# Optimization experiments

Measured on AMD Instinct MI355X. Metric: run time of the kernel, lower is better.

Reference implementation:

```python
import jax, jax.numpy as jnp
import numpy as np

D_IN = 64      # num_in_features
D_OUT = 64     # num_out_features
H = 512        # neurons_per_layer
M = 64         # num_meta_in_features
META_OUT = D_IN * H + H + H * D_OUT + D_OUT  # 66112
B = 2048


def setup_inputs() -> dict:
    key = jax.random.key(0)
    k1, k2, k3 = jax.random.split(key, 3)
    x = jax.random.normal(k1, (B, D_IN + M), dtype=jnp.float32)
    # xavier-normal-ish init for the two hypernet linears, zero biases
    W_in = jax.random.normal(k2, (H, M), dtype=jnp.float32) * jnp.sqrt(2.0 / (H + M))
    b_in = jnp.zeros((H,), dtype=jnp.float32)
    W_out = jax.random.normal(k3, (META_OUT, H), dtype=jnp.float32) * jnp.sqrt(2.0 / (META_OUT + H))
    b_out = jnp.zeros((META_OUT,), dtype=jnp.float32)
    return {"x": x, "W_in": W_in, "b_in": b_in, "W_out": W_out, "b_out": b_out}


def reference(x, W_in, b_in, W_out, b_out):
    real = x[:, :D_IN]            # [B, D_IN]
    meta = x[:, D_IN:]            # [B, M]
    h = jax.nn.elu(meta @ W_in.T + b_in)          # [B, H]
    gen = h @ W_out.T + b_out                     # [B, META_OUT]
    base = D_IN * H
    l_in_w = gen[:, :base].reshape(-1, D_IN, H)   # [B, D_IN, H]
    l_in_b = gen[:, base:base + H]                # [B, H]
    base += H
    add = H * D_OUT
    l_out_w = gen[:, base:base + add].reshape(-1, H, D_OUT)  # [B, H, D_OUT]
    l_out_b = gen[:, base + add:]                 # [B, D_OUT]
    # tensordot(real, l_in_w, dims=([1],[1])).diagonal(0,1).T == per-sample matvec
    y = jax.nn.elu(jnp.einsum('bi,bih->bh', real, l_in_w) + l_in_b)
    out = jnp.einsum('bh,bho->bo', y, l_out_w) + l_out_b
    return out
```

## Files before the change

kernel.cpp:

```cpp
#include <hip/hip_runtime.h>
#include <hip/hip_bf16.h>
#include <stdint.h>

#define B_N   2048
#define XW    128
#define KDIM  512
#define NROWS_W   66112
#define NROWS_PAD 66560

typedef __bf16 v8bf  __attribute__((ext_vector_type(8)));
typedef float  f32x4 __attribute__((ext_vector_type(4)));

__device__ __forceinline__ unsigned short f2bf(float f) {
    uint32_t u = __float_as_uint(f);
    u += 0x7FFF + ((u >> 16) & 1);
    return (unsigned short)(u >> 16);
}
__device__ __forceinline__ float elu1(float v) {
    return v > 0.0f ? v : expm1f(v);
}
__device__ __forceinline__ void gload_lds16(const void* g, void* l) {
    __builtin_amdgcn_global_load_lds(
        (const __attribute__((address_space(1))) unsigned int*)g,
        (__attribute__((address_space(3))) unsigned int*)l, 16, 0, 0);
}

__global__ void k_h(const float* __restrict__ x, const float* __restrict__ W_in,
                    const float* __restrict__ b_in, unsigned short* __restrict__ hb) {
    int idx = blockIdx.x * 256 + threadIdx.x;
    int b = idx >> 9, j = idx & 511;
    const float4* xm = (const float4*)(x + (size_t)b * XW + 64);
    const float4* wr = (const float4*)(W_in + (size_t)j * 64);
    float acc = 0.f;
#pragma unroll
    for (int q = 0; q < 16; ++q) {
        float4 a = xm[q], w = wr[q];
        acc += a.x * w.x + a.y * w.y + a.z * w.z + a.w * w.w;
    }
    acc = elu1(acc + b_in[j]);
    hb[idx] = f2bf(acc);
}

__global__ void k_conv(const float* __restrict__ Wf, unsigned short* __restrict__ Wb) {
    size_t c = (size_t)blockIdx.x * 256 + threadIdx.x;
    size_t row = c >> 6; int kk = (int)(c & 63);
    union { uint4 v; unsigned short u[8]; } o;
    o.v = (uint4){0, 0, 0, 0};
    if (row < NROWS_W) {
        const float* wp = Wf + row * KDIM + kk * 8;
        float4 w0 = *(const float4*)wp, w1 = *(const float4*)(wp + 4);
        o.u[0] = f2bf(w0.x); o.u[1] = f2bf(w0.y); o.u[2] = f2bf(w0.z); o.u[3] = f2bf(w0.w);
        o.u[4] = f2bf(w1.x); o.u[5] = f2bf(w1.y); o.u[6] = f2bf(w1.z); o.u[7] = f2bf(w1.w);
    }
    *(uint4*)(Wb + c * 8) = o.v;
}

template<int MODE>
__global__ __launch_bounds__(256, 2)
void k_pgemm(const unsigned short* __restrict__ hb,
             const unsigned short* __restrict__ Wb,
             const float* __restrict__ scaleSrc,
             float* __restrict__ outAcc) {
    constexpr int NP   = MODE ? 129 : 130;
    constexpr int OUTW = MODE ? 64 : 512;
    constexpr int SCW  = MODE ? 18 : 9;

    __shared__ char smem[65536 + SCW * 128 * 4];
    char* As = smem;
    char* Bs = smem + 32768;
    float* sc = (float*)(smem + 65536);

    const int tid = threadIdx.x;
    const int m0  = blockIdx.x * 128;
    const int nh  = blockIdx.y;
    const int s   = blockIdx.z;
    const int pBeg = (NP * s) >> 4;
    const int pEnd = (NP * (s + 1)) >> 4;
    const int halfS = (MODE == 0 && pBeg >= 65) ? 1 : 0;
    const int iBeg  = pBeg - halfS * 65;

    const int wid = tid >> 6, l = tid & 63;
    const int lr = l & 15, lg = l >> 4;
    const int wm = wid >> 1, wn = wid & 1;

    for (int c = tid; c < SCW * 128; c += 256) {
        int jj = c >> 7, row = c & 127;
        float v = 1.0f;
        if (MODE == 0) {
            int i = iBeg + jj;
            if (i < 64) v = scaleSrc[(size_t)(m0 + row) * XW + i];
        } else {
            int g = (pBeg + (jj >> 1)) * 4 + nh * 2 + (jj & 1);
            if (g < 512) v = scaleSrc[(size_t)(m0 + row) * KDIM + g];
        }
        sc[c] = v;
    }

    int aB[4], aX[4], bB[4], bX[4];
#pragma unroll
    for (int q = 0; q < 4; ++q) {
        int ra = wm * 64 + q * 16 + lr;
        aB[q] = ra * 256; aX[q] = ra & 7;
        int rb = wn * 64 + q * 16 + lr;
        bB[q] = rb * 128; bX[q] = rb & 7;
    }

    f32x4 accP[4][4], accO[4][4];
#pragma unroll
    for (int mi = 0; mi < 4; ++mi)
#pragma unroll
        for (int ni = 0; ni < 4; ++ni) {
            accP[mi][ni] = (f32x4){0.f, 0.f, 0.f, 0.f};
            accO[mi][ni] = (f32x4){0.f, 0.f, 0.f, 0.f};
        }

    for (int kq = 0; kq < 4; ++kq) {
#pragma unroll
        for (int q = 0; q < 8; ++q) {
            int c = q * 256 + tid;
            int row = c >> 4, kk = c & 15;
            uint4 v = *(const uint4*)(hb + (size_t)(m0 + row) * KDIM + kq * 128 + kk * 8);
            *(uint4*)(As + row * 256 + ((kk ^ (row & 7)) << 4)) = v;
        }
        auto stageB = [&](int buf, int p, int k0c) {
            int wrow = MODE ? (33280 + p * 256 + nh * 128)
                            : ((p - halfS * 65) * 512 + halfS * 256 + nh * 128);
            const int rsub = tid >> 3;
            const int sl = (tid & 7) ^ (rsub & 7);
            const unsigned short* src0 = Wb + (size_t)(wrow + rsub) * KDIM
                                       + kq * 128 + k0c * 64 + sl * 8;
            char* dst0 = Bs + buf * 16384 + tid * 16;
#pragma unroll
            for (int q = 0; q < 4; ++q)
                gload_lds16(src0 + (size_t)q * 32 * KDIM, dst0 + q * 4096);
        };
        stageB(0, pBeg, 0);
        __syncthreads();
        int cur = 0;
        for (int p = pBeg; p < pEnd; ++p) {
#pragma unroll
            for (int k0 = 0; k0 < 2; ++k0) {
                const bool last = (p == pEnd - 1) && (k0 == 1);
                if (!last) {
                    stageB(cur ^ 1, k0 ? p + 1 : p, k0 ^ 1);
                    asm volatile("s_waitcnt vmcnt(4)" ::: "memory");
                } else {
                    asm volatile("s_waitcnt vmcnt(0)" ::: "memory");
                }
                __builtin_amdgcn_s_barrier();
                asm volatile("" ::: "memory");
                char* Bbuf = Bs + cur * 16384;
                __builtin_amdgcn_s_setprio(1);
#pragma unroll
                for (int ks = 0; ks < 2; ++ks) {
                    v8bf af[4], bfr[4];
                    const int sA = k0 * 8 + ks * 4 + lg;
                    const int sB = ks * 4 + lg;
#pragma unroll
                    for (int mi = 0; mi < 4; ++mi)
                        af[mi] = *(const v8bf*)(As + aB[mi] + ((sA ^ aX[mi]) << 4));
#pragma unroll
                    for (int ni = 0; ni < 4; ++ni)
                        bfr[ni] = *(const v8bf*)(Bbuf + bB[ni] + ((sB ^ bX[ni]) << 4));
#pragma unroll
                    for (int mi = 0; mi < 4; ++mi)
#pragma unroll
                        for (int ni = 0; ni < 4; ++ni)
                            accP[mi][ni] = __builtin_amdgcn_mfma_f32_16x16x32_bf16(
                                af[mi], bfr[ni], accP[mi][ni], 0, 0, 0);
                }
                __builtin_amdgcn_s_setprio(0);
                if (k0 == 1) {
                    int jj = MODE ? ((p - pBeg) * 2 + wn) : (p - pBeg);
                    const f32x4* scv = (const f32x4*)(sc + jj * 128);
#pragma unroll
                    for (int mi = 0; mi < 4; ++mi) {
                        f32x4 sv = scv[wm * 16 + mi * 4 + lg];
#pragma unroll
                        for (int ni = 0; ni < 4; ++ni) {
                            accO[mi][ni] += sv * accP[mi][ni];
                            accP[mi][ni] = (f32x4){0.f, 0.f, 0.f, 0.f};
                        }
                    }
                }
                asm volatile("" ::: "memory");
                __builtin_amdgcn_s_barrier();
                cur ^= 1;
            }
        }
    }
#pragma unroll
    for (int mi = 0; mi < 4; ++mi)
#pragma unroll
        for (int ni = 0; ni < 4; ++ni)
#pragma unroll
            for (int r = 0; r < 4; ++r) {
                int row = wm * 64 + mi * 16 + lg * 4 + r;
                int col = MODE ? (ni * 16 + lr)
                               : (halfS * 256 + nh * 128 + wn * 64 + ni * 16 + lr);
                atomicAdd(outAcc + (size_t)(m0 + row) * OUTW + col, accO[mi][ni][r]);
            }
}

__global__ void k_fin_y(const float* __restrict__ ypre, const float* __restrict__ x,
                        const float* __restrict__ b_out, float* __restrict__ y) {
    int idx = blockIdx.x * 256 + threadIdx.x;
    int b = idx >> 9, hh = idx & 511;
    float acc = ypre[idx] + b_out[32768 + hh];
    const float* xr = x + (size_t)b * XW;
#pragma unroll 8
    for (int i = 0; i < 64; ++i)
        acc += xr[i] * b_out[i * 512 + hh];
    y[idx] = elu1(acc);
}

__global__ void k_fin_out(const float* __restrict__ y, const float* __restrict__ b_out,
                          float* __restrict__ out) {
    int idx = blockIdx.x * 256 + threadIdx.x;
    int b = idx >> 6, o = idx & 63;
    float acc = out[idx] + b_out[66048 + o];
    const float* yr = y + (size_t)b * 512;
#pragma unroll 8
    for (int hh = 0; hh < 512; ++hh)
        acc += yr[hh] * b_out[33280 + hh * 64 + o];
    out[idx] = acc;
}

extern "C" void kernel_launch(void* const* d_in, const int* in_sizes, int n_in,
                              void* d_out, int out_size, void* d_ws, size_t ws_size,
                              hipStream_t stream) {
    const float* x     = (const float*)d_in[0];
    const float* W_in  = (const float*)d_in[1];
    const float* b_in  = (const float*)d_in[2];
    const float* W_out = (const float*)d_in[3];
    const float* b_out = (const float*)d_in[4];
    float* out = (float*)d_out;

    char* ws = (char*)d_ws;
    unsigned short* hb = (unsigned short*)ws;
    float* ypre        = (float*)(ws + (2u << 20));
    float* yv          = (float*)(ws + (6u << 20));
    unsigned short* Wb = (unsigned short*)(ws + (10u << 20));

    hipMemsetAsync(ypre, 0, (size_t)B_N * 512 * 4, stream);
    hipMemsetAsync(out,  0, (size_t)B_N * 64 * 4, stream);

    k_h<<<(B_N * 512) / 256, 256, 0, stream>>>(x, W_in, b_in, hb);
    k_conv<<<(NROWS_PAD * KDIM / 8) / 256, 256, 0, stream>>>(W_out, Wb);

    k_pgemm<0><<<dim3(16, 2, 16), 256, 0, stream>>>(hb, Wb, x, ypre);

    k_fin_y<<<(B_N * 512) / 256, 256, 0, stream>>>(ypre, x, b_out, yv);

    k_pgemm<1><<<dim3(16, 2, 16), 256, 0, stream>>>(hb, Wb, yv, out);

    k_fin_out<<<(B_N * 64) / 256, 256, 0, stream>>>(yv, b_out, out);
}
```

Measured before the change: 284.4 us.

## Hold A fragments in registers, enlarge M tile, fold bias terms into init kernels

The projected GEMM now uses 512-thread blocks covering 256 rows. Each wave loads its A (h) fragments straight from global memory into registers once per k-quarter instead of staging them through LDS. This halves LDS use and doubles reuse of each streamed W tile. The grid is flattened to 256 blocks with a custom mapping of split index to block. The memsets and the two finalize kernels are replaced by init kernels that write the bias contributions before the atomics, and ELU is applied on the fly when scales are loaded and inside k_init_out. The cost is higher register pressure and direct global A loads without LDS swizzling.

```diff
diff --git a/kernel.cpp b/kernel.cpp
--- a/kernel.cpp
+++ b/kernel.cpp
@@ -55,8 +55,32 @@
     *(uint4*)(Wb + c * 8) = o.v;
 }
 
+__global__ void k_init_ypre(const float* __restrict__ x, const float* __restrict__ b_out,
+                            float* __restrict__ ypre) {
+    int idx = blockIdx.x * 256 + threadIdx.x;
+    int b = idx >> 9, hh = idx & 511;
+    float acc = b_out[32768 + hh];
+    const float* xr = x + (size_t)b * XW;
+#pragma unroll 8
+    for (int i = 0; i < 64; ++i)
+        acc += xr[i] * b_out[i * 512 + hh];
+    ypre[idx] = acc;
+}
+
+__global__ void k_init_out(const float* __restrict__ ypre, const float* __restrict__ b_out,
+                           float* __restrict__ out) {
+    int idx = blockIdx.x * 256 + threadIdx.x;
+    int b = idx >> 6, o = idx & 63;
+    float acc = b_out[66048 + o];
+    const float* yr = ypre + (size_t)b * 512;
+#pragma unroll 4
+    for (int hh = 0; hh < 512; ++hh)
+        acc += elu1(yr[hh]) * b_out[33280 + hh * 64 + o];
+    out[idx] = acc;
+}
+
 template<int MODE>
-__global__ __launch_bounds__(256, 2)
+__global__ __launch_bounds__(512, 2)
 void k_pgemm(const unsigned short* __restrict__ hb,
              const unsigned short* __restrict__ Wb,
              const float* __restrict__ scaleSrc,
@@ -65,42 +89,42 @@
     constexpr int OUTW = MODE ? 64 : 512;
     constexpr int SCW  = MODE ? 18 : 9;
 
-    __shared__ char smem[65536 + SCW * 128 * 4];
-    char* As = smem;
-    char* Bs = smem + 32768;
-    float* sc = (float*)(smem + 65536);
-
-    const int tid = threadIdx.x;
-    const int m0  = blockIdx.x * 128;
-    const int nh  = blockIdx.y;
-    const int s   = blockIdx.z;
+    __shared__ char smem[32768 + SCW * 256 * 4];
+    char* Bs = smem;
+    float* sc = (float*)(smem + 32768);
+
+    const int lid = blockIdx.x;
+    const int s   = (lid & 7) * 2 + (lid >> 7);
+    const int inner = (lid >> 3) & 15;
+    const int m0  = (inner & 7) * 256;
+    const int nh  = inner >> 3;
+
     const int pBeg = (NP * s) >> 4;
     const int pEnd = (NP * (s + 1)) >> 4;
     const int halfS = (MODE == 0 && pBeg >= 65) ? 1 : 0;
     const int iBeg  = pBeg - halfS * 65;
 
+    const int tid = threadIdx.x;
     const int wid = tid >> 6, l = tid & 63;
     const int lr = l & 15, lg = l >> 4;
     const int wm = wid >> 1, wn = wid & 1;
 
-    for (int c = tid; c < SCW * 128; c += 256) {
-        int jj = c >> 7, row = c & 127;
+    for (int c = tid; c < SCW * 256; c += 512) {
+        int jj = c >> 8, row = c & 255;
         float v = 1.0f;
         if (MODE == 0) {
             int i = iBeg + jj;
             if (i < 64) v = scaleSrc[(size_t)(m0 + row) * XW + i];
         } else {
             int g = (pBeg + (jj >> 1)) * 4 + nh * 2 + (jj & 1);
-            if (g < 512) v = scaleSrc[(size_t)(m0 + row) * KDIM + g];
+            if (g < 512) v = elu1(scaleSrc[(size_t)(m0 + row) * KDIM + g]);
         }
         sc[c] = v;
     }
 
-    int aB[4], aX[4], bB[4], bX[4];
+    int bB[4], bX[4];
 #pragma unroll
     for (int q = 0; q < 4; ++q) {
-        int ra = wm * 64 + q * 16 + lr;
-        aB[q] = ra * 256; aX[q] = ra & 7;
         int rb = wn * 64 + q * 16 + lr;
         bB[q] = rb * 128; bX[q] = rb & 7;
     }
@@ -115,13 +139,6 @@
         }
 
     for (int kq = 0; kq < 4; ++kq) {
-#pragma unroll
-        for (int q = 0; q < 8; ++q) {
-            int c = q * 256 + tid;
-            int row = c >> 4, kk = c & 15;
-            uint4 v = *(const uint4*)(hb + (size_t)(m0 + row) * KDIM + kq * 128 + kk * 8);
-            *(uint4*)(As + row * 256 + ((kk ^ (row & 7)) << 4)) = v;
-        }
         auto stageB = [&](int buf, int p, int k0c) {
             int wrow = MODE ? (33280 + p * 256 + nh * 128)
                             : ((p - halfS * 65) * 512 + halfS * 256 + nh * 128);
@@ -131,11 +148,21 @@
                                        + kq * 128 + k0c * 64 + sl * 8;
             char* dst0 = Bs + buf * 16384 + tid * 16;
 #pragma unroll
-            for (int q = 0; q < 4; ++q)
-                gload_lds16(src0 + (size_t)q * 32 * KDIM, dst0 + q * 4096);
+            for (int q = 0; q < 2; ++q)
+                gload_lds16(src0 + (size_t)q * 64 * KDIM, dst0 + q * 8192);
         };
+
         stageB(0, pBeg, 0);
-        __syncthreads();
+
+        const unsigned short* abase = hb + (size_t)(m0 + wm * 64 + lr) * KDIM
+                                    + kq * 128 + lg * 8;
+        v8bf areg[4][4];
+#pragma unroll
+        for (int mi = 0; mi < 4; ++mi)
+#pragma unroll
+            for (int kk2 = 0; kk2 < 4; ++kk2)
+                areg[mi][kk2] = *(const v8bf*)(abase + mi * 16 * KDIM + kk2 * 32);
+
         int cur = 0;
         for (int p = pBeg; p < pEnd; ++p) {
 #pragma unroll
@@ -143,7 +170,7 @@
                 const bool last = (p == pEnd - 1) && (k0 == 1);
                 if (!last) {
                     stageB(cur ^ 1, k0 ? p + 1 : p, k0 ^ 1);
-                    asm volatile("s_waitcnt vmcnt(4)" ::: "memory");
+                    asm volatile("s_waitcnt vmcnt(2)" ::: "memory");
                 } else {
                     asm volatile("s_waitcnt vmcnt(0)" ::: "memory");
                 }
@@ -153,12 +180,8 @@
                 __builtin_amdgcn_s_setprio(1);
 #pragma unroll
                 for (int ks = 0; ks < 2; ++ks) {
-                    v8bf af[4], bfr[4];
-                    const int sA = k0 * 8 + ks * 4 + lg;
+                    v8bf bfr[4];
                     const int sB = ks * 4 + lg;
-#pragma unroll
-                    for (int mi = 0; mi < 4; ++mi)
-                        af[mi] = *(const v8bf*)(As + aB[mi] + ((sA ^ aX[mi]) << 4));
 #pragma unroll
                     for (int ni = 0; ni < 4; ++ni)
                         bfr[ni] = *(const v8bf*)(Bbuf + bB[ni] + ((sB ^ bX[ni]) << 4));
@@ -167,12 +190,12 @@
 #pragma unroll
                         for (int ni = 0; ni < 4; ++ni)
                             accP[mi][ni] = __builtin_amdgcn_mfma_f32_16x16x32_bf16(
-                                af[mi], bfr[ni], accP[mi][ni], 0, 0, 0);
+                                areg[mi][k0 * 2 + ks], bfr[ni], accP[mi][ni], 0, 0, 0);
                 }
                 __builtin_amdgcn_s_setprio(0);
                 if (k0 == 1) {
                     int jj = MODE ? ((p - pBeg) * 2 + wn) : (p - pBeg);
-                    const f32x4* scv = (const f32x4*)(sc + jj * 128);
+                    const f32x4* scv = (const f32x4*)(sc + jj * 256);
 #pragma unroll
                     for (int mi = 0; mi < 4; ++mi) {
                         f32x4 sv = scv[wm * 16 + mi * 4 + lg];
@@ -202,30 +225,6 @@
             }
 }
 
-__global__ void k_fin_y(const float* __restrict__ ypre, const float* __restrict__ x,
-                        const float* __restrict__ b_out, float* __restrict__ y) {
-    int idx = blockIdx.x * 256 + threadIdx.x;
-    int b = idx >> 9, hh = idx & 511;
-    float acc = ypre[idx] + b_out[32768 + hh];
-    const float* xr = x + (size_t)b * XW;
-#pragma unroll 8
-    for (int i = 0; i < 64; ++i)
-        acc += xr[i] * b_out[i * 512 + hh];
-    y[idx] = elu1(acc);
-}
-
-__global__ void k_fin_out(const float* __restrict__ y, const float* __restrict__ b_out,
-                          float* __restrict__ out) {
-    int idx = blockIdx.x * 256 + threadIdx.x;
-    int b = idx >> 6, o = idx & 63;
-    float acc = out[idx] + b_out[66048 + o];
-    const float* yr = y + (size_t)b * 512;
-#pragma unroll 8
-    for (int hh = 0; hh < 512; ++hh)
-        acc += yr[hh] * b_out[33280 + hh * 64 + o];
-    out[idx] = acc;
-}
-
 extern "C" void kernel_launch(void* const* d_in, const int* in_sizes, int n_in,
                               void* d_out, int out_size, void* d_ws, size_t ws_size,
                               hipStream_t stream) {
@@ -239,20 +238,16 @@
     char* ws = (char*)d_ws;
     unsigned short* hb = (unsigned short*)ws;
     float* ypre        = (float*)(ws + (2u << 20));
-    float* yv          = (float*)(ws + (6u << 20));
-    unsigned short* Wb = (unsigned short*)(ws + (10u << 20));
-
-    hipMemsetAsync(ypre, 0, (size_t)B_N * 512 * 4, stream);
-    hipMemsetAsync(out,  0, (size_t)B_N * 64 * 4, stream);
+    unsigned short* Wb = (unsigned short*)(ws + (6u << 20));
 
     k_h<<<(B_N * 512) / 256, 256, 0, stream>>>(x, W_in, b_in, hb);
     k_conv<<<(NROWS_PAD * KDIM / 8) / 256, 256, 0, stream>>>(W_out, Wb);
 
-    k_pgemm<0><<<dim3(16, 2, 16), 256, 0, stream>>>(hb, Wb, x, ypre);
-
-    k_fin_y<<<(B_N * 512) / 256, 256, 0, stream>>>(ypre, x, b_out, yv);
-
-    k_pgemm<1><<<dim3(16, 2, 16), 256, 0, stream>>>(hb, Wb, yv, out);
-
-    k_fin_out<<<(B_N * 64) / 256, 256, 0, stream>>>(yv, b_out, out);
-}
+    k_init_ypre<<<(B_N * 512) / 256, 256, 0, stream>>>(x, b_out, ypre);
+
+    k_pgemm<0><<<256, 512, 0, stream>>>(hb, Wb, x, ypre);
+
+    k_init_out<<<(B_N * 64) / 256, 256, 0, stream>>>(ypre, b_out, out);
+
+    k_pgemm<1><<<256, 512, 0, stream>>>(hb, Wb, ypre, out);
+}
```

New measurement: 371.0 us. +30.4%, slower.
